# Kernel optimization log

Hardware: AMD Instinct MI355X
Metric: run time of the kernel (lower is better)

Reference implementation:

```python
import jax, jax.numpy as jnp
import numpy as np

B, S, D, H = 512, 64, 1024, 16  # seq_len=64 fixed by Reshape([-1,8,8,d_model])
DH = D // H


def setup_inputs() -> dict:
    key = jax.random.key(0)
    ks = jax.random.split(key, 5)
    w_scale = 0.02  # keep pre-softmax logits / activations in a sane range
    return {
        "x": jax.random.normal(ks[0], (B, S, D), jnp.float32),
        "wq_w": jax.random.normal(ks[1], (D, D), jnp.float32) * w_scale,
        "wq_b": jnp.zeros((D,), jnp.float32),
        "wk_w": jax.random.normal(ks[2], (D, D), jnp.float32) * w_scale,
        "wk_b": jnp.zeros((D,), jnp.float32),
        "wv_w": jax.random.normal(ks[3], (D, D), jnp.float32) * w_scale,
        "wv_b": jnp.zeros((D,), jnp.float32),
        "wo_w": jax.random.normal(ks[4], (D, D), jnp.float32) * w_scale,
        "wo_b": jnp.zeros((D,), jnp.float32),
    }


def _split_heads(t):
    # [B, S, D] -> [B, H, S, DH]
    b, s, _ = t.shape
    return t.reshape(b, s, H, DH).transpose(0, 2, 1, 3)


def reference(x, wq_w, wq_b, wk_w, wk_b, wv_w, wv_b, wo_w, wo_b):
    b, s, d = x.shape
    q = _split_heads(x @ wq_w + wq_b)
    k = _split_heads(x @ wk_w + wk_b)
    v = _split_heads(x @ wv_w + wv_b)
    # NOTE: original scales by sqrt(d_model), not sqrt(depth)
    scores = jnp.einsum("bhqd,bhkd->bhqk", q, k) / jnp.sqrt(jnp.float32(d))
    # original 'padding mask': (scores == 0) * 1e-9 added to scores
    scores = scores + (scores == 0).astype(scores.dtype) * 1e-9
    attn = jax.nn.softmax(scores, axis=-1)
    ctx = jnp.einsum("bhqk,bhkd->bhqd", attn, v)  # [B, H, S, DH]
    ctx = ctx.transpose(0, 2, 1, 3).reshape(b, s, d)  # [B, S, D]
    # keras Dense(..., activation='gelu') uses exact (erf) gelu by default
    out = jax.nn.gelu(ctx @ wo_w + wo_b, approximate=False)
    # Reshape([-1, 8, 8, D]) then squeeze -> [B, 8, 8, D]
    return out.reshape(b, 8, 8, d)
```

## Files before the change

### kernel.cpp

```cpp
#include <hip/hip_runtime.h>
#include <cstdint>
#include <math.h>

typedef float f32x4 __attribute__((ext_vector_type(4)));
typedef __bf16 bf16x8 __attribute__((ext_vector_type(8)));
typedef unsigned short u16x8 __attribute__((ext_vector_type(8)));
typedef unsigned short u16x4 __attribute__((ext_vector_type(4)));

typedef __attribute__((address_space(1))) const void* gas_cvptr;
typedef __attribute__((address_space(3))) void* las_vptr;

#define WAITV8 asm volatile("s_waitcnt vmcnt(8)" ::: "memory")
#define WAITV4 asm volatile("s_waitcnt vmcnt(4)" ::: "memory")
#define WAITV0 asm volatile("s_waitcnt vmcnt(0)" ::: "memory")
#define WAITL0 asm volatile("s_waitcnt lgkmcnt(0)" ::: "memory")
#define BAR()  __builtin_amdgcn_s_barrier()

__device__ __forceinline__ unsigned short f32_to_bf16(float f) {
  uint32_t u = __builtin_bit_cast(uint32_t, f);
  u += 0x7FFFu + ((u >> 16) & 1u);
  return (unsigned short)(u >> 16);
}

__device__ __forceinline__ bf16x8 ld_bf16x8(const unsigned short* p) {
  return __builtin_bit_cast(bf16x8, *(const u16x8*)p);
}

__global__ void cvt_x(const float* __restrict__ x, unsigned short* __restrict__ xb, int n4) {
  int stride = gridDim.x * blockDim.x;
  for (int i = blockIdx.x * blockDim.x + threadIdx.x; i < n4; i += stride) {
    float4 v = ((const float4*)x)[i];
    u16x4 o = { f32_to_bf16(v.x), f32_to_bf16(v.y), f32_to_bf16(v.z), f32_to_bf16(v.w) };
    ((u16x4*)xb)[i] = o;
  }
}

__global__ void cvt_w(const float* __restrict__ wq, const float* __restrict__ wk,
                      const float* __restrict__ wv, const float* __restrict__ wo,
                      unsigned short* __restrict__ wqkvT, unsigned short* __restrict__ woT) {
  const int z = blockIdx.z;
  const float* __restrict__ w = (z == 0) ? wq : (z == 1) ? wk : (z == 2) ? wv : wo;
  unsigned short* __restrict__ out = (z < 3) ? (wqkvT + (size_t)z * 1024 * 1024) : woT;
  __shared__ float tile[64][65];
  const int r0 = blockIdx.y * 64;
  const int c0 = blockIdx.x * 64;
  const int t = threadIdx.x;
#pragma unroll
  for (int i = 0; i < 4; i++) {
    int row = (t >> 4) + i * 16;
    int col = (t & 15) * 4;
    float4 v = *(const float4*)&w[(size_t)(r0 + row) * 1024 + c0 + col];
    tile[row][col] = v.x; tile[row][col + 1] = v.y;
    tile[row][col + 2] = v.z; tile[row][col + 3] = v.w;
  }
  __syncthreads();
#pragma unroll
  for (int i = 0; i < 2; i++) {
    int nr = (t >> 3) + i * 32;
    int kc = (t & 7) * 8;
    u16x8 o;
#pragma unroll
    for (int j = 0; j < 8; j++) o[j] = f32_to_bf16(tile[kc + j][nr]);
    *(u16x8*)&out[(size_t)(c0 + nr) * 1024 + r0 + kc] = o;
  }
}

template <int EPI>
__global__ __launch_bounds__(512, 2) void gemm256(
    const unsigned short* __restrict__ A, const unsigned short* __restrict__ Bt,
    const float* __restrict__ b0, const float* __restrict__ b1, const float* __restrict__ b2,
    unsigned short* __restrict__ Qb, unsigned short* __restrict__ Kb, unsigned short* __restrict__ Vb,
    float* __restrict__ Out, int Ncols, int K) {
  __shared__ __align__(16) unsigned short As[4][256][32];
  __shared__ __align__(16) unsigned short Bs[4][256][32];
  const int NT = K >> 5;
  const int nb = Ncols >> 8;
  const int nwg = gridDim.x;
  const int cpx = nwg >> 3;
  const int bid = blockIdx.x;
  const int wg = (bid & 7) * cpx + (bid >> 3);
  const int tm = wg / nb, tn = wg % nb;
  const int rowBase = tm << 8, colBase = tn << 8;
  const int t = threadIdx.x;
  const int lane = t & 63;
  const int w = t >> 6;
  const int li = lane & 15, lg = lane >> 4;
  const int wm = w >> 2, wn = w & 3;
  const int aRow0 = wm * 128;
  const int bRow0 = wn * 64;

  const int c0 = t, c1 = t + 512;
  const int r0s = c0 >> 2, s0s = c0 & 3;
  const int r1s = c1 >> 2, s1s = c1 & 3;
  const unsigned short* gA0 = A + (size_t)(rowBase + r0s) * K + s0s * 8;
  const unsigned short* gA1 = A + (size_t)(rowBase + r1s) * K + s1s * 8;
  const unsigned short* gB0 = Bt + (size_t)(colBase + r0s) * K + s0s * 8;
  const unsigned short* gB1 = Bt + (size_t)(colBase + r1s) * K + s1s * 8;

#define STAGE_A(tile_) do { int b_ = (tile_) & 3; int kt_ = (tile_) << 5;                     \
    __builtin_amdgcn_global_load_lds((gas_cvptr)(gA0 + kt_),                                  \
        (las_vptr)(&As[b_][0][0] + c0 * 8), 16, 0, 0);                                        \
    __builtin_amdgcn_global_load_lds((gas_cvptr)(gA1 + kt_),                                  \
        (las_vptr)(&As[b_][0][0] + c1 * 8), 16, 0, 0); } while (0)
#define STAGE_B(tile_) do { int b_ = (tile_) & 3; int kt_ = (tile_) << 5;                     \
    __builtin_amdgcn_global_load_lds((gas_cvptr)(gB0 + kt_),                                  \
        (las_vptr)(&Bs[b_][0][0] + c0 * 8), 16, 0, 0);                                        \
    __builtin_amdgcn_global_load_lds((gas_cvptr)(gB1 + kt_),                                  \
        (las_vptr)(&Bs[b_][0][0] + c1 * 8), 16, 0, 0); } while (0)

  STAGE_A(0); STAGE_B(0);
  STAGE_A(1); STAGE_B(1);
  STAGE_A(2); STAGE_B(2);
  WAITV8;
  BAR();

  f32x4 acc[8][4] = {};
  bf16x8 af[4], bfr[4];

  for (int tt = 0; tt < NT; ++tt) {
    const unsigned short* ab = &As[tt & 3][0][0];
    const unsigned short* bb = &Bs[tt & 3][0][0];
#pragma unroll
    for (int m = 0; m < 4; m++) af[m] = ld_bf16x8(ab + (aRow0 + m * 16 + li) * 32 + lg * 8);
#pragma unroll
    for (int n = 0; n < 4; n++) bfr[n] = ld_bf16x8(bb + (bRow0 + n * 16 + li) * 32 + lg * 8);
    if (tt + 3 < NT) STAGE_A(tt + 3);
    BAR();
    WAITL0;
    __builtin_amdgcn_s_setprio(1);
#pragma unroll
    for (int m = 0; m < 4; m++)
#pragma unroll
      for (int n = 0; n < 4; n++)
        acc[m][n] = __builtin_amdgcn_mfma_f32_16x16x32_bf16(af[m], bfr[n], acc[m][n], 0, 0, 0);
    __builtin_amdgcn_s_setprio(0);
    BAR();
#pragma unroll
    for (int m = 0; m < 4; m++)
      af[m] = ld_bf16x8(ab + (aRow0 + 64 + m * 16 + li) * 32 + lg * 8);
    if (tt + 3 < NT) STAGE_B(tt + 3);
    BAR();
    WAITL0;
    __builtin_amdgcn_s_setprio(1);
#pragma unroll
    for (int m = 0; m < 4; m++)
#pragma unroll
      for (int n = 0; n < 4; n++)
        acc[4 + m][n] = __builtin_amdgcn_mfma_f32_16x16x32_bf16(af[m], bfr[n], acc[4 + m][n], 0, 0, 0);
    __builtin_amdgcn_s_setprio(0);
    if (tt <= NT - 4)      WAITV8;
    else if (tt == NT - 3) WAITV4;
    else                   WAITV0;
    BAR();
  }
#undef STAGE_A
#undef STAGE_B

  if (EPI == 0) {
    const int part = colBase >> 10;
    const float* __restrict__ bias = (part == 0) ? b0 : (part == 1) ? b1 : b2;
    unsigned short* __restrict__ dst = (part == 0) ? Qb : (part == 1) ? Kb : Vb;
#pragma unroll
    for (int mi = 0; mi < 8; mi++) {
      const int rowb = rowBase + aRow0 + mi * 16 + lg * 4;
#pragma unroll
      for (int r = 0; r < 4; r++) {
        const int row = rowb + r;
        const int b = row >> 6, s = row & 63;
#pragma unroll
        for (int n = 0; n < 4; n++) {
          const int col = colBase + bRow0 + n * 16 + li;
          const int within = col & 1023;
          const int h = within >> 6, dh = within & 63;
          float v = acc[mi][n][r] + bias[within];
          dst[(size_t)((b * 16 + h) * 64 + s) * 64 + dh] = f32_to_bf16(v);
        }
      }
    }
  } else {
#pragma unroll
    for (int mi = 0; mi < 8; mi++) {
      const int rowb = rowBase + aRow0 + mi * 16 + lg * 4;
#pragma unroll
      for (int r = 0; r < 4; r++) {
#pragma unroll
        for (int n = 0; n < 4; n++) {
          const int col = colBase + bRow0 + n * 16 + li;
          float v = acc[mi][n][r] + b0[col];
          v = 0.5f * v * (1.0f + erff(v * 0.70710678118654752f));
          Out[(size_t)(rowb + r) * 1024 + col] = v;
        }
      }
    }
  }
}

__global__ __launch_bounds__(256) void attn(
    const unsigned short* __restrict__ Qb, const unsigned short* __restrict__ Kb,
    const unsigned short* __restrict__ Vb, unsigned short* __restrict__ ctx) {
  __shared__ __align__(16) unsigned short Qs[64][72];
  __shared__ __align__(16) unsigned short Ks[64][72];
  __shared__ __align__(16) unsigned short Vt[64][72];
  __shared__ __align__(16) unsigned short Ps[64][72];
  const int bh = blockIdx.x;
  const int b = bh >> 4, h = bh & 15;
  const int t = threadIdx.x, lane = t & 63, w = t >> 6;
  const int li = lane & 15, lg = lane >> 4;
  const unsigned short* __restrict__ Qg = Qb + (size_t)bh * 4096;
  const unsigned short* __restrict__ Kg = Kb + (size_t)bh * 4096;
  const unsigned short* __restrict__ Vg = Vb + (size_t)bh * 4096;

#pragma unroll
  for (int i = 0; i < 2; i++) {
    const int c = t + i * 256;
    const int row = c >> 3, col8 = (c & 7) * 8;
    *(u16x8*)&Qs[row][col8] = *(const u16x8*)&Qg[row * 64 + col8];
    *(u16x8*)&Ks[row][col8] = *(const u16x8*)&Kg[row * 64 + col8];
    u16x8 v = *(const u16x8*)&Vg[row * 64 + col8];
#pragma unroll
    for (int j = 0; j < 8; j++) Vt[col8 + j][row] = v[j];
  }
  __syncthreads();

  f32x4 sc[4] = {};
#pragma unroll
  for (int ks = 0; ks < 2; ks++) {
    bf16x8 qa = ld_bf16x8(&Qs[w * 16 + li][ks * 32 + lg * 8]);
#pragma unroll
    for (int n = 0; n < 4; n++) {
      bf16x8 kf = ld_bf16x8(&Ks[n * 16 + li][ks * 32 + lg * 8]);
      sc[n] = __builtin_amdgcn_mfma_f32_16x16x32_bf16(qa, kf, sc[n], 0, 0, 0);
    }
  }

#pragma unroll
  for (int r = 0; r < 4; r++) {
    float v0 = sc[0][r] * 0.03125f, v1 = sc[1][r] * 0.03125f;
    float v2 = sc[2][r] * 0.03125f, v3 = sc[3][r] * 0.03125f;
    float mx = fmaxf(fmaxf(v0, v1), fmaxf(v2, v3));
#pragma unroll
    for (int off = 1; off < 16; off <<= 1) mx = fmaxf(mx, __shfl_xor(mx, off, 64));
    float e0 = __expf(v0 - mx), e1 = __expf(v1 - mx);
    float e2 = __expf(v2 - mx), e3 = __expf(v3 - mx);
    float sum = e0 + e1 + e2 + e3;
#pragma unroll
    for (int off = 1; off < 16; off <<= 1) sum += __shfl_xor(sum, off, 64);
    float is = 1.0f / sum;
    const int q = w * 16 + lg * 4 + r;
    Ps[q][0 * 16 + li] = f32_to_bf16(e0 * is);
    Ps[q][1 * 16 + li] = f32_to_bf16(e1 * is);
    Ps[q][2 * 16 + li] = f32_to_bf16(e2 * is);
    Ps[q][3 * 16 + li] = f32_to_bf16(e3 * is);
  }
  __syncthreads();

  f32x4 oc[4] = {};
#pragma unroll
  for (int ks = 0; ks < 2; ks++) {
    bf16x8 pa = ld_bf16x8(&Ps[w * 16 + li][ks * 32 + lg * 8]);
#pragma unroll
    for (int n = 0; n < 4; n++) {
      bf16x8 vf = ld_bf16x8(&Vt[n * 16 + li][ks * 32 + lg * 8]);
      oc[n] = __builtin_amdgcn_mfma_f32_16x16x32_bf16(pa, vf, oc[n], 0, 0, 0);
    }
  }
#pragma unroll
  for (int n = 0; n < 4; n++)
#pragma unroll
    for (int r = 0; r < 4; r++)
      ctx[(size_t)(b * 64 + w * 16 + lg * 4 + r) * 1024 + h * 64 + n * 16 + li] =
          f32_to_bf16(oc[n][r]);
}

extern "C" void kernel_launch(void* const* d_in, const int* in_sizes, int n_in,
                              void* d_out, int out_size, void* d_ws, size_t ws_size,
                              hipStream_t stream) {
  const float* x  = (const float*)d_in[0];
  const float* wq = (const float*)d_in[1];
  const float* bq = (const float*)d_in[2];
  const float* wk = (const float*)d_in[3];
  const float* bk = (const float*)d_in[4];
  const float* wv = (const float*)d_in[5];
  const float* bv = (const float*)d_in[6];
  const float* wo = (const float*)d_in[7];
  const float* bo = (const float*)d_in[8];
  float* out = (float*)d_out;

  const int D = 1024;
  const int M = in_sizes[0] / D;

  char* ws = (char*)d_ws;
  unsigned short* xb    = (unsigned short*)ws;
  unsigned short* wqkvT = (unsigned short*)(ws + (size_t)M * 1024 * 2);
  unsigned short* woT   = wqkvT + (size_t)3 * 1024 * 1024;
  unsigned short* Qb    = woT + (size_t)1024 * 1024;
  unsigned short* Kb    = Qb + (size_t)M * 1024;
  unsigned short* Vb    = Kb + (size_t)M * 1024;
  unsigned short* ctx   = xb;

  cvt_x<<<2048, 256, 0, stream>>>(x, xb, M * D / 4);
  cvt_w<<<dim3(16, 16, 4), 256, 0, stream>>>(wq, wk, wv, wo, wqkvT, woT);
  gemm256<0><<<(M / 256) * (3072 / 256), 512, 0, stream>>>(
      xb, wqkvT, bq, bk, bv, Qb, Kb, Vb, nullptr, 3072, 1024);
  attn<<<(M / 64) * 16, 256, 0, stream>>>(Qb, Kb, Vb, ctx);
  gemm256<1><<<(M / 256) * (1024 / 256), 512, 0, stream>>>(
      ctx, woT, bo, nullptr, nullptr, nullptr, nullptr, nullptr, out, 1024, 1024);
}
```

Measured before the change: 428.5 us.

## Restructure GEMM mainloop into 8-phase schedule with K=64 tiles and swizzled LDS

The GEMM kernel now uses K=64 tiles with two LDS buffers instead of four K=32 buffers. LDS columns are XOR-swizzled to avoid bank conflicts. Each iteration is split into four MFMA quadrants, and the next tile's half-tile global-to-LDS loads are interleaved between them, with sched_barrier and priority hints controlling issue order. The aim is better overlap of memory and MFMA work and fewer barriers per unit of compute. In exchange the kernel holds more fragment registers and runs a shallower prefetch pipeline.

```diff
diff --git a/kernel.cpp b/kernel.cpp
--- a/kernel.cpp
+++ b/kernel.cpp
@@ -10,11 +10,13 @@
 typedef __attribute__((address_space(1))) const void* gas_cvptr;
 typedef __attribute__((address_space(3))) void* las_vptr;
 
-#define WAITV8 asm volatile("s_waitcnt vmcnt(8)" ::: "memory")
-#define WAITV4 asm volatile("s_waitcnt vmcnt(4)" ::: "memory")
+#define WAITV2 asm volatile("s_waitcnt vmcnt(2)" ::: "memory")
 #define WAITV0 asm volatile("s_waitcnt vmcnt(0)" ::: "memory")
 #define WAITL0 asm volatile("s_waitcnt lgkmcnt(0)" ::: "memory")
+#define SB()   __builtin_amdgcn_sched_barrier(0)
 #define BAR()  __builtin_amdgcn_s_barrier()
+#define PRIO1() __builtin_amdgcn_s_setprio(1)
+#define PRIO0() __builtin_amdgcn_s_setprio(0)
 
 __device__ __forceinline__ unsigned short f32_to_bf16(float f) {
   uint32_t u = __builtin_bit_cast(uint32_t, f);
@@ -66,14 +68,14 @@
 }
 
 template <int EPI>
-__global__ __launch_bounds__(512, 2) void gemm256(
+__global__ __launch_bounds__(512, 2) void gemm8p(
     const unsigned short* __restrict__ A, const unsigned short* __restrict__ Bt,
-    const float* __restrict__ b0, const float* __restrict__ b1, const float* __restrict__ b2,
+    const float* __restrict__ b0p, const float* __restrict__ b1p, const float* __restrict__ b2p,
     unsigned short* __restrict__ Qb, unsigned short* __restrict__ Kb, unsigned short* __restrict__ Vb,
     float* __restrict__ Out, int Ncols, int K) {
-  __shared__ __align__(16) unsigned short As[4][256][32];
-  __shared__ __align__(16) unsigned short Bs[4][256][32];
-  const int NT = K >> 5;
+  __shared__ __align__(16) unsigned short As[2][256][64];
+  __shared__ __align__(16) unsigned short Bs[2][256][64];
+  const int NT = K >> 6;
   const int nb = Ncols >> 8;
   const int nwg = gridDim.x;
   const int cpx = nwg >> 3;
@@ -86,90 +88,139 @@
   const int w = t >> 6;
   const int li = lane & 15, lg = lane >> 4;
   const int wm = w >> 2, wn = w & 3;
-  const int aRow0 = wm * 128;
-  const int bRow0 = wn * 64;
+  const int aBase = wm << 7;
+  const int bBase = wn << 6;
+  const int pcb0 = (lg ^ (li & 7)) << 3;
+  const int pcb1 = ((4 + lg) ^ (li & 7)) << 3;
 
   const int c0 = t, c1 = t + 512;
-  const int r0s = c0 >> 2, s0s = c0 & 3;
-  const int r1s = c1 >> 2, s1s = c1 & 3;
-  const unsigned short* gA0 = A + (size_t)(rowBase + r0s) * K + s0s * 8;
-  const unsigned short* gA1 = A + (size_t)(rowBase + r1s) * K + s1s * 8;
-  const unsigned short* gB0 = Bt + (size_t)(colBase + r0s) * K + s0s * 8;
-  const unsigned short* gB1 = Bt + (size_t)(colBase + r1s) * K + s1s * 8;
-
-#define STAGE_A(tile_) do { int b_ = (tile_) & 3; int kt_ = (tile_) << 5;                     \
-    __builtin_amdgcn_global_load_lds((gas_cvptr)(gA0 + kt_),                                  \
-        (las_vptr)(&As[b_][0][0] + c0 * 8), 16, 0, 0);                                        \
-    __builtin_amdgcn_global_load_lds((gas_cvptr)(gA1 + kt_),                                  \
-        (las_vptr)(&As[b_][0][0] + c1 * 8), 16, 0, 0); } while (0)
-#define STAGE_B(tile_) do { int b_ = (tile_) & 3; int kt_ = (tile_) << 5;                     \
-    __builtin_amdgcn_global_load_lds((gas_cvptr)(gB0 + kt_),                                  \
-        (las_vptr)(&Bs[b_][0][0] + c0 * 8), 16, 0, 0);                                        \
-    __builtin_amdgcn_global_load_lds((gas_cvptr)(gB1 + kt_),                                  \
-        (las_vptr)(&Bs[b_][0][0] + c1 * 8), 16, 0, 0); } while (0)
-
-  STAGE_A(0); STAGE_B(0);
-  STAGE_A(1); STAGE_B(1);
-  STAGE_A(2); STAGE_B(2);
-  WAITV8;
+  const int r0s = c0 >> 3, r1s = c1 >> 3;
+  const size_t off0 = (size_t)r0s * K + (((c0 & 7) ^ (r0s & 7)) << 3);
+  const size_t off1 = (size_t)r1s * K + (((c1 & 7) ^ (r1s & 7)) << 3);
+  const unsigned short* srcA = A + (size_t)rowBase * K;
+  const unsigned short* srcB = Bt + (size_t)colBase * K;
+
+#define GLDS(s_, d_) __builtin_amdgcn_global_load_lds((gas_cvptr)(s_), (las_vptr)(d_), 16, 0, 0)
+#define STAGE_A(b_, h_, t_) do {                                                   \
+    const unsigned short* s_ = srcA + (size_t)(h_) * 128 * K + ((t_) << 6);        \
+    unsigned short* d_ = &As[b_][(h_) * 128][0];                                   \
+    GLDS(s_ + off0, d_ + c0 * 8); GLDS(s_ + off1, d_ + c1 * 8); } while (0)
+#define STAGE_B(b_, h_, t_) do {                                                   \
+    const unsigned short* s_ = srcB + (size_t)(h_) * 128 * K + ((t_) << 6);        \
+    unsigned short* d_ = &Bs[b_][(h_) * 128][0];                                   \
+    GLDS(s_ + off0, d_ + c0 * 8); GLDS(s_ + off1, d_ + c1 * 8); } while (0)
+
+  STAGE_A(0, 0, 0); STAGE_A(0, 1, 0); STAGE_B(0, 0, 0); STAGE_B(0, 1, 0);
+  STAGE_A(1, 0, 1);
+  WAITV2;
   BAR();
 
   f32x4 acc[8][4] = {};
-  bf16x8 af[4], bfr[4];
+  bf16x8 a0[8], a1[8], b0f[4], b1f[4];
 
   for (int tt = 0; tt < NT; ++tt) {
-    const unsigned short* ab = &As[tt & 3][0][0];
-    const unsigned short* bb = &Bs[tt & 3][0][0];
-#pragma unroll
-    for (int m = 0; m < 4; m++) af[m] = ld_bf16x8(ab + (aRow0 + m * 16 + li) * 32 + lg * 8);
-#pragma unroll
-    for (int n = 0; n < 4; n++) bfr[n] = ld_bf16x8(bb + (bRow0 + n * 16 + li) * 32 + lg * 8);
-    if (tt + 3 < NT) STAGE_A(tt + 3);
-    BAR();
-    WAITL0;
-    __builtin_amdgcn_s_setprio(1);
-#pragma unroll
-    for (int m = 0; m < 4; m++)
-#pragma unroll
-      for (int n = 0; n < 4; n++)
-        acc[m][n] = __builtin_amdgcn_mfma_f32_16x16x32_bf16(af[m], bfr[n], acc[m][n], 0, 0, 0);
-    __builtin_amdgcn_s_setprio(0);
-    BAR();
-#pragma unroll
-    for (int m = 0; m < 4; m++)
-      af[m] = ld_bf16x8(ab + (aRow0 + 64 + m * 16 + li) * 32 + lg * 8);
-    if (tt + 3 < NT) STAGE_B(tt + 3);
-    BAR();
-    WAITL0;
-    __builtin_amdgcn_s_setprio(1);
-#pragma unroll
-    for (int m = 0; m < 4; m++)
-#pragma unroll
-      for (int n = 0; n < 4; n++)
-        acc[4 + m][n] = __builtin_amdgcn_mfma_f32_16x16x32_bf16(af[m], bfr[n], acc[4 + m][n], 0, 0, 0);
-    __builtin_amdgcn_s_setprio(0);
-    if (tt <= NT - 4)      WAITV8;
-    else if (tt == NT - 3) WAITV4;
-    else                   WAITV0;
+    const int buf = tt & 1;
+    const unsigned short* ab = &As[buf][0][0];
+    const unsigned short* bb = &Bs[buf][0][0];
+#pragma unroll
+    for (int m = 0; m < 4; m++) {
+      const unsigned short* rp = ab + (aBase + m * 16 + li) * 64;
+      a0[m * 2] = ld_bf16x8(rp + pcb0);
+      a0[m * 2 + 1] = ld_bf16x8(rp + pcb1);
+    }
+#pragma unroll
+    for (int n = 0; n < 2; n++) {
+      const unsigned short* rp = bb + (bBase + n * 16 + li) * 64;
+      b0f[n * 2] = ld_bf16x8(rp + pcb0);
+      b0f[n * 2 + 1] = ld_bf16x8(rp + pcb1);
+    }
+    if (tt + 1 < NT) STAGE_A(buf ^ 1, 1, tt + 1);
+    BAR();
+    WAITL0; SB();
+    PRIO1();
+#pragma unroll
+    for (int ks = 0; ks < 2; ks++)
+#pragma unroll
+      for (int m = 0; m < 4; m++)
+#pragma unroll
+        for (int n = 0; n < 2; n++)
+          acc[m][n] = __builtin_amdgcn_mfma_f32_16x16x32_bf16(a0[m * 2 + ks], b0f[n * 2 + ks],
+                                                              acc[m][n], 0, 0, 0);
+    PRIO0();
+    BAR();
+#pragma unroll
+    for (int n = 0; n < 2; n++) {
+      const unsigned short* rp = bb + (bBase + 32 + n * 16 + li) * 64;
+      b1f[n * 2] = ld_bf16x8(rp + pcb0);
+      b1f[n * 2 + 1] = ld_bf16x8(rp + pcb1);
+    }
+    if (tt + 1 < NT) STAGE_B(buf ^ 1, 0, tt + 1);
+    BAR();
+    WAITL0; SB();
+    PRIO1();
+#pragma unroll
+    for (int ks = 0; ks < 2; ks++)
+#pragma unroll
+      for (int m = 0; m < 4; m++)
+#pragma unroll
+        for (int n = 0; n < 2; n++)
+          acc[m][2 + n] = __builtin_amdgcn_mfma_f32_16x16x32_bf16(a0[m * 2 + ks], b1f[n * 2 + ks],
+                                                                  acc[m][2 + n], 0, 0, 0);
+    PRIO0();
+    BAR();
+#pragma unroll
+    for (int m = 0; m < 4; m++) {
+      const unsigned short* rp = ab + (aBase + 64 + m * 16 + li) * 64;
+      a1[m * 2] = ld_bf16x8(rp + pcb0);
+      a1[m * 2 + 1] = ld_bf16x8(rp + pcb1);
+    }
+    if (tt + 1 < NT) STAGE_B(buf ^ 1, 1, tt + 1);
+    BAR();
+    WAITL0; SB();
+    PRIO1();
+#pragma unroll
+    for (int ks = 0; ks < 2; ks++)
+#pragma unroll
+      for (int m = 0; m < 4; m++)
+#pragma unroll
+        for (int n = 0; n < 2; n++)
+          acc[4 + m][2 + n] = __builtin_amdgcn_mfma_f32_16x16x32_bf16(a1[m * 2 + ks], b1f[n * 2 + ks],
+                                                                      acc[4 + m][2 + n], 0, 0, 0);
+    PRIO0();
+    BAR();
+    if (tt + 2 < NT) STAGE_A(buf, 0, tt + 2);
+    if (tt >= NT - 2) { WAITV0; } else { WAITV2; }
+    BAR();
+    PRIO1();
+#pragma unroll
+    for (int ks = 0; ks < 2; ks++)
+#pragma unroll
+      for (int m = 0; m < 4; m++)
+#pragma unroll
+        for (int n = 0; n < 2; n++)
+          acc[4 + m][n] = __builtin_amdgcn_mfma_f32_16x16x32_bf16(a1[m * 2 + ks], b0f[n * 2 + ks],
+                                                                  acc[4 + m][n], 0, 0, 0);
+    PRIO0();
     BAR();
   }
 #undef STAGE_A
 #undef STAGE_B
+#undef GLDS
 
   if (EPI == 0) {
     const int part = colBase >> 10;
-    const float* __restrict__ bias = (part == 0) ? b0 : (part == 1) ? b1 : b2;
+    const float* __restrict__ bias = (part == 0) ? b0p : (part == 1) ? b1p : b2p;
     unsigned short* __restrict__ dst = (part == 0) ? Qb : (part == 1) ? Kb : Vb;
 #pragma unroll
     for (int mi = 0; mi < 8; mi++) {
-      const int rowb = rowBase + aRow0 + mi * 16 + lg * 4;
+      const int rowb = rowBase + aBase + mi * 16 + lg * 4;
 #pragma unroll
       for (int r = 0; r < 4; r++) {
         const int row = rowb + r;
         const int b = row >> 6, s = row & 63;
 #pragma unroll
         for (int n = 0; n < 4; n++) {
-          const int col = colBase + bRow0 + n * 16 + li;
+          const int col = colBase + bBase + n * 16 + li;
           const int within = col & 1023;
           const int h = within >> 6, dh = within & 63;
           float v = acc[mi][n][r] + bias[within];
@@ -180,13 +231,13 @@
   } else {
 #pragma unroll
     for (int mi = 0; mi < 8; mi++) {
-      const int rowb = rowBase + aRow0 + mi * 16 + lg * 4;
+      const int rowb = rowBase + aBase + mi * 16 + lg * 4;
 #pragma unroll
       for (int r = 0; r < 4; r++) {
 #pragma unroll
         for (int n = 0; n < 4; n++) {
-          const int col = colBase + bRow0 + n * 16 + li;
-          float v = acc[mi][n][r] + b0[col];
+          const int col = colBase + bBase + n * 16 + li;
+          float v = acc[mi][n][r] + b0p[col];
           v = 0.5f * v * (1.0f + erff(v * 0.70710678118654752f));
           Out[(size_t)(rowb + r) * 1024 + col] = v;
         }
@@ -300,9 +351,9 @@
 
   cvt_x<<<2048, 256, 0, stream>>>(x, xb, M * D / 4);
   cvt_w<<<dim3(16, 16, 4), 256, 0, stream>>>(wq, wk, wv, wo, wqkvT, woT);
-  gemm256<0><<<(M / 256) * (3072 / 256), 512, 0, stream>>>(
+  gemm8p<0><<<(M / 256) * (3072 / 256), 512, 0, stream>>>(
       xb, wqkvT, bq, bk, bv, Qb, Kb, Vb, nullptr, 3072, 1024);
   attn<<<(M / 64) * 16, 256, 0, stream>>>(Qb, Kb, Vb, ctx);
-  gemm256<1><<<(M / 256) * (1024 / 256), 512, 0, stream>>>(
+  gemm8p<1><<<(M / 256) * (1024 / 256), 512, 0, stream>>>(
       ctx, woT, bo, nullptr, nullptr, nullptr, nullptr, nullptr, out, 1024, 1024);
 }
```

Result: no change. 422.1 us (-1.5%).
